# Optimization experiments

Measured on AMD Instinct MI355X. Metric: run time of the kernel, lower is better.

The kernel has to match this reference:

```python
import jax, jax.numpy as jnp
import numpy as np
from functools import partial

C_IN = 32
KT = 10  # 3*3 taps + bias


def avgpool(x, k):
    B, C, H, W = x.shape
    return x.reshape(B, C, H // k, k, W // k, k).mean(axis=(3, 5))


def conv3x3(x, w, b):
    out = jax.lax.conv_general_dilated(
        x, w, window_strides=(1, 1), padding=[(1, 1), (1, 1)],
        dimension_numbers=("NCHW", "OIHW", "NCHW"))
    return out + b[None, :, None, None]


def conv1x1(x, w, b):
    # w: [O, C, 1, 1]
    return jnp.einsum("bchw,oc->bohw", x, w[:, :, 0, 0]) + b[None, :, None, None]


def predictor(x, w1, b1, w2, b2):
    return x + conv3x3(jax.nn.leaky_relu(conv3x3(x, w1, b1), 0.01), w2, b2)


def flying_conv(x, weight, bias):
    # x: [B,C,H,W]; weight: [B,C,Hb,Wb,9]; bias: [B,C,Hb,Wb]; 8x8 blocks
    B, C, H, W = x.shape
    Hb, Wb = H // 8, W // 8
    xp = jnp.pad(x, ((0, 0), (0, 0), (1, 1), (1, 1)))
    out = jnp.broadcast_to(bias[:, :, :, None, :, None], (B, C, Hb, 8, Wb, 8))
    for k in range(9):
        di, dj = k // 3, k % 3
        xs = xp[:, :, di:di + H, dj:dj + W].reshape(B, C, Hb, 8, Wb, 8)
        out = out + xs * weight[:, :, :, None, :, None, k]
    return out.reshape(B, C, H, W)


def setup_inputs() -> dict:
    key = jax.random.key(0)
    ks = jax.random.split(key, 5)
    B, C, H, W = 4, C_IN, 512, 512
    x = jax.random.normal(ks[0], (B, C, H, W), dtype=jnp.float32)
    pa_w = jax.random.normal(ks[1], (4, 2, C, C, 3, 3), dtype=jnp.float32) * 0.05
    pa_b = jnp.zeros((4, 2, C), dtype=jnp.float32)
    exp_w = jax.random.normal(ks[2], (C * KT, C, 1, 1), dtype=jnp.float32) * 0.05
    exp_b = jnp.zeros((C * KT,), dtype=jnp.float32)
    pw_w = jax.random.normal(ks[3], (C, C, 1, 1), dtype=jnp.float32) * 0.1
    pw_b = jnp.zeros((C,), dtype=jnp.float32)
    return {"x": x, "pa_w": pa_w, "pa_b": pa_b, "exp_w": exp_w,
            "exp_b": exp_b, "pw_w": pw_w, "pw_b": pw_b}


def reference(x, pa_w, pa_b, exp_w, exp_b, pw_w, pw_b):
    B, C, H, W = x.shape
    feat = avgpool(x, 4)  # H/4
    for i in range(4):
        feat = predictor(feat, pa_w[i, 0], pa_b[i, 0], pa_w[i, 1], pa_b[i, 1])
        if i == 1:
            feat = avgpool(feat, 2)  # -> H/8
    wmap = conv1x1(feat, exp_w, exp_b)  # [B, C*10, Hb, Wb]
    Hb, Wb = H // 8, W // 8
    wmap = jnp.tanh(wmap.reshape(B, C, KT, Hb, Wb).transpose(0, 1, 3, 4, 2))
    weight, bias = wmap[..., :9], wmap[..., 9]
    out = flying_conv(x, weight, bias)
    return conv1x1(out, pw_w, pw_b)
```

## Files before the change

kernel.cpp:

```cpp
#include <hip/hip_runtime.h>


#define BATCH 4
#define NCH 32
#define CS128 17680
#define SP128 136
#define CS64 4752
#define SP64 72

__device__ __forceinline__ float fast_tanh(float s) {
  float e = __expf(2.f * s);
  return fmaf(-2.f, __builtin_amdgcn_rcpf(e + 1.f), 1.f);
}

__global__ void zero_kernel(float* __restrict__ p) {
  int i = blockIdx.x * 256 + threadIdx.x;
  *reinterpret_cast<float4*>(p + (size_t)i * 4) = make_float4(0.f, 0.f, 0.f, 0.f);
}

__global__ void prep_kernel(const float* __restrict__ pa_w, const float* __restrict__ exp_w,
                            const float* __restrict__ pw_w, float* __restrict__ wt,
                            float* __restrict__ ewt, float* __restrict__ pwt) {
  int i = blockIdx.x * 256 + threadIdx.x;
  if (i < 73728) {
    int tap = i % 9; int t = i / 9;
    int ci = t & 31; t >>= 5;
    int co = t & 31; int layer = t >> 5;
    wt[((layer * 32 + ci) * 9 + tap) * 32 + co] = pa_w[i];
  } else if (i < 83968) {
    int j = i - 73728; int ci = j & 31; int o = j >> 5;
    ewt[ci * 320 + o] = exp_w[j];
  } else if (i < 84992) {
    int j = i - 83968; int c = j & 31; int o = j >> 5;
    pwt[c * 32 + o] = pw_w[j];
  }
}

__global__ void avgpool4_kernel(const float* __restrict__ x, float* __restrict__ outp) {
  int idx = blockIdx.x * 256 + threadIdx.x;
  if (idx >= BATCH * NCH * 128 * 128) return;
  int ow = idx & 127; int t = idx >> 7; int oh = t & 127; int bc = t >> 7;
  const float* src = x + ((size_t)(bc * 512 + oh * 4)) * 512 + ow * 4;
  float s = 0.f;
#pragma unroll
  for (int r = 0; r < 4; r++) {
    float4 v = *reinterpret_cast<const float4*>(src + (size_t)r * 512);
    s += v.x + v.y + v.z + v.w;
  }
  outp[(size_t)bc * CS128 + (size_t)(oh + 1) * SP128 + ow + 4] = s * 0.0625f;
}

__global__ void avgpool2_kernel(const float* __restrict__ inp, float* __restrict__ outp) {
  int idx = blockIdx.x * 256 + threadIdx.x;
  if (idx >= BATCH * NCH * 64 * 64) return;
  int ow = idx & 63; int t = idx >> 6; int oh = t & 63; int bc = t >> 6;
  const float* sp = inp + (size_t)bc * CS128 + (size_t)(2 * oh + 1) * SP128 + 2 * ow + 4;
  float2 a = *reinterpret_cast<const float2*>(sp);
  float2 b = *reinterpret_cast<const float2*>(sp + SP128);
  outp[(size_t)bc * CS64 + (size_t)(oh + 1) * SP64 + ow + 4] = (a.x + a.y + b.x + b.y) * 0.25f;
}

template <int HS, int SP, int CS, int NCO, bool RELU, bool RES>
__global__ __launch_bounds__(256) void conv3x3d_kernel(
    const float* __restrict__ in, const float* __restrict__ wt,
    const float* __restrict__ bias, const float* __restrict__ res,
    float* __restrict__ out) {
  constexpr int TILES = HS / 16;
  constexpr int GROUPS = 32 / NCO;
  int blk = blockIdx.x;
  int g = blk % GROUPS; int rest = blk / GROUPS;
  int b = rest / (TILES * TILES); int t = rest % (TILES * TILES);
  int ty = t / TILES, tx = t % TILES;
  int og = g * NCO;
  int px = threadIdx.x & 15, py = threadIdx.x >> 4;
  int gy = ty * 16 + py, gx = tx * 16 + px;
  size_t pix = (size_t)(gy + 1) * SP + gx + 4;
  const float* inb = in + (size_t)b * 32 * CS + pix;

  float acc[NCO];
#pragma unroll
  for (int o = 0; o < NCO; o++) acc[o] = bias[og + o];

  for (int ci = 0; ci < 32; ci++) {
    const float* p = inb + (size_t)ci * CS;
    float v[9];
    v[0] = p[-SP - 1]; v[1] = p[-SP]; v[2] = p[-SP + 1];
    v[3] = p[-1];      v[4] = p[0];   v[5] = p[1];
    v[6] = p[SP - 1];  v[7] = p[SP];  v[8] = p[SP + 1];
    const float* wr = wt + ci * 288 + og;
#pragma unroll
    for (int tap = 0; tap < 9; tap++) {
      const float* wrow = wr + tap * 32;
#pragma unroll
      for (int o = 0; o < NCO; o++)
        acc[o] = fmaf(v[tap], wrow[o], acc[o]);
    }
  }

  float* ob = out + (size_t)b * 32 * CS + (size_t)og * CS + pix;
  const float* rb = RES ? (res + (size_t)b * 32 * CS + (size_t)og * CS + pix) : nullptr;
#pragma unroll
  for (int o = 0; o < NCO; o++) {
    float r2 = acc[o];
    if (RELU) r2 = r2 > 0.f ? r2 : 0.01f * r2;
    if (RES) r2 += rb[(size_t)o * CS];
    ob[(size_t)o * CS] = r2;
  }
}

__global__ __launch_bounds__(256) void expander_kernel(
    const float* __restrict__ feat, const float* __restrict__ ewt,
    const float* __restrict__ eb, float* __restrict__ wmap) {
  int idx = blockIdx.x * 256 + threadIdx.x;
  int wq = idx & 15; int t = idx >> 4;
  int o = t % 320; int rest = t / 320;
  int hb = rest & 63; int b = rest >> 6;
  const float* fp = feat + (size_t)b * 32 * CS64 + (size_t)(hb + 1) * SP64 + 4 + wq * 4;
  float s0 = eb[o];
  float s1 = s0, s2 = s0, s3 = s0;
#pragma unroll 8
  for (int ci = 0; ci < 32; ci++) {
    float4 f = *reinterpret_cast<const float4*>(fp + (size_t)ci * CS64);
    float wv = ewt[ci * 320 + o];
    s0 = fmaf(f.x, wv, s0); s1 = fmaf(f.y, wv, s1);
    s2 = fmaf(f.z, wv, s2); s3 = fmaf(f.w, wv, s3);
  }
  float4 r;
  r.x = fast_tanh(s0); r.y = fast_tanh(s1);
  r.z = fast_tanh(s2); r.w = fast_tanh(s3);
  *reinterpret_cast<float4*>(wmap + (size_t)((b * 64 + hb) * 320 + o) * 64 + wq * 4) = r;
}

__global__ __launch_bounds__(256, 4) void fused_fly_pw_kernel(
    const float* __restrict__ x, const float* __restrict__ wmap,
    const float* __restrict__ pwt, const float* __restrict__ pw_b,
    float* __restrict__ out, int b0) {
  __shared__ float s_w[8][322];
  __shared__ float s_x[8][10][68];
  int blk = blockIdx.x;
  int wtile = blk & 7; int t = blk >> 3; int hb = t & 63; int b = b0 + (t >> 6);
  int tid = threadIdx.x;

  const float* wsrc = wmap + (size_t)(b * 64 + hb) * 320 * 64 + wtile * 8;
#pragma unroll
  for (int j = 0; j < 10; j++) {
    int idx = j * 256 + tid;
    int tap = idx >> 3, wb8 = idx & 7;
    s_w[wb8][tap] = wsrc[(size_t)tap * 64 + wb8];
  }

  int cp = tid & 31, row = tid >> 5;
  int h = hb * 8 + row;
  int w0 = wtile * 64 + cp * 2;
  int wbl = cp >> 2;
  int h0 = hb * 8;
  int gc0 = wtile * 64 - 1;
  const float* xb = x + (size_t)b * 32 * 262144;

  float2 acc[32];
#pragma unroll
  for (int o = 0; o < 32; o++) {
    float bv = pw_b[o];
    acc[o].x = bv; acc[o].y = bv;
  }

  for (int g = 0; g < 4; g++) {
    __syncthreads();
    const float* xg = xb + (size_t)(g * 8) * 262144;
    for (int e = tid; e < 5280; e += 256) {
      int ch = e / 660; int r2 = e - ch * 660;
      int rr = r2 / 66; int cl = r2 - rr * 66;
      int gy = h0 - 1 + rr, gx = gc0 + cl;
      float v = 0.f;
      if (gy >= 0 && gy < 512 && gx >= 0 && gx < 512)
        v = xg[(size_t)ch * 262144 + (size_t)gy * 512 + gx];
      s_x[ch][rr][cl] = v;
    }
    __syncthreads();

#pragma unroll
    for (int c8 = 0; c8 < 8; c8++) {
      int c = g * 8 + c8;
      const float2* wr2 = reinterpret_cast<const float2*>(&s_w[wbl][c * 10]);
      float2 w01 = wr2[0], w23 = wr2[1], w45 = wr2[2], w67 = wr2[3], w89 = wr2[4];
      float wv[9];
      wv[0] = w01.x; wv[1] = w01.y; wv[2] = w23.x;
      wv[3] = w23.y; wv[4] = w45.x; wv[5] = w45.y;
      wv[6] = w67.x; wv[7] = w67.y; wv[8] = w89.x;
      float fly0 = w89.y, fly1 = w89.y;

#pragma unroll
      for (int di = 0; di < 3; di++) {
        const float2* rp = reinterpret_cast<const float2*>(&s_x[c8][row + di][cp * 2]);
        float2 a = rp[0], bb = rp[1];
        float wa = wv[di * 3 + 0], wb_ = wv[di * 3 + 1], wc = wv[di * 3 + 2];
        fly0 = fmaf(a.x, wa, fly0); fly0 = fmaf(a.y, wb_, fly0); fly0 = fmaf(bb.x, wc, fly0);
        fly1 = fmaf(a.y, wa, fly1); fly1 = fmaf(bb.x, wb_, fly1); fly1 = fmaf(bb.y, wc, fly1);
      }
      const float* prow = pwt + c * 32;
#pragma unroll
      for (int o = 0; o < 32; o++) {
        float pw = prow[o];
        acc[o].x = fmaf(fly0, pw, acc[o].x);
        acc[o].y = fmaf(fly1, pw, acc[o].y);
      }
    }
  }
  float* ob = out + (size_t)b * 32 * 262144 + (size_t)h * 512 + w0;
#pragma unroll
  for (int o = 0; o < 32; o++)
    *reinterpret_cast<float2*>(ob + (size_t)o * 262144) = acc[o];
}

extern "C" void kernel_launch(void* const* d_in, const int* in_sizes, int n_in,
                              void* d_out, int out_size, void* d_ws, size_t ws_size,
                              hipStream_t stream) {
  const float* x     = (const float*)d_in[0];
  const float* pa_w  = (const float*)d_in[1];
  const float* pa_b  = (const float*)d_in[2];
  const float* exp_w = (const float*)d_in[3];
  const float* exp_b = (const float*)d_in[4];
  const float* pw_w  = (const float*)d_in[5];
  const float* pw_b  = (const float*)d_in[6];
  float* out = (float*)d_out;
  float* ws  = (float*)d_ws;

  float* feat0p = ws;
  float* tmpAp  = feat0p + 2263040;
  float* feat1p = tmpAp + 2263040;
  float* wmap   = feat1p + 608256;
  float* tmpBp  = wmap;
  float* wt     = wmap + 5242880;
  float* ewt    = wt + 73728;
  float* pwt    = ewt + 10240;

  hipLaunchKernelGGL(zero_kernel, dim3(5608), dim3(256), 0, stream, ws);
  hipLaunchKernelGGL(prep_kernel, dim3(332), dim3(256), 0, stream, pa_w, exp_w, pw_w, wt, ewt, pwt);
  hipLaunchKernelGGL(avgpool4_kernel, dim3(8192), dim3(256), 0, stream, x, feat0p);

  for (int i = 0; i < 2; i++) {
    const float* w1 = wt + (size_t)(i * 2 + 0) * 9216;
    const float* b1 = pa_b + (i * 2 + 0) * 32;
    const float* w2 = wt + (size_t)(i * 2 + 1) * 9216;
    const float* b2 = pa_b + (i * 2 + 1) * 32;
    hipLaunchKernelGGL((conv3x3d_kernel<128, SP128, CS128, 8, true, false>),
                       dim3(1024), dim3(256), 0, stream, feat0p, w1, b1, nullptr, tmpAp);
    hipLaunchKernelGGL((conv3x3d_kernel<128, SP128, CS128, 8, false, true>),
                       dim3(1024), dim3(256), 0, stream, tmpAp, w2, b2, feat0p, feat0p);
  }

  hipLaunchKernelGGL(avgpool2_kernel, dim3(2048), dim3(256), 0, stream, feat0p, feat1p);

  for (int i = 2; i < 4; i++) {
    const float* w1 = wt + (size_t)(i * 2 + 0) * 9216;
    const float* b1 = pa_b + (i * 2 + 0) * 32;
    const float* w2 = wt + (size_t)(i * 2 + 1) * 9216;
    const float* b2 = pa_b + (i * 2 + 1) * 32;
    hipLaunchKernelGGL((conv3x3d_kernel<64, SP64, CS64, 4, true, false>),
                       dim3(512), dim3(256), 0, stream, feat1p, w1, b1, nullptr, tmpBp);
    hipLaunchKernelGGL((conv3x3d_kernel<64, SP64, CS64, 4, false, true>),
                       dim3(512), dim3(256), 0, stream, tmpBp, w2, b2, feat1p, feat1p);
  }

  hipLaunchKernelGGL(expander_kernel, dim3(5120), dim3(256), 0, stream, feat1p, ewt, exp_b, wmap);

  hipLaunchKernelGGL(fused_fly_pw_kernel, dim3(1024), dim3(256), 0, stream,
                     x, wmap, pwt, pw_b, out, 0);
  hipLaunchKernelGGL(fused_fly_pw_kernel, dim3(1024), dim3(256), 0, stream,
                     x, wmap, pwt, pw_b, out, 2);
}
```

Baseline: 380.4 us.

## Halve per-thread work in conv and fused flying-conv kernels, merge batch launches

```diff
diff --git a/kernel.cpp b/kernel.cpp
--- a/kernel.cpp
+++ b/kernel.cpp
@@ -81,6 +81,7 @@
 #pragma unroll
   for (int o = 0; o < NCO; o++) acc[o] = bias[og + o];
 
+#pragma unroll 2
   for (int ci = 0; ci < 32; ci++) {
     const float* p = inb + (size_t)ci * CS;
     float v[9];
@@ -131,43 +132,40 @@
   *reinterpret_cast<float4*>(wmap + (size_t)((b * 64 + hb) * 320 + o) * 64 + wq * 4) = r;
 }
 
-__global__ __launch_bounds__(256, 4) void fused_fly_pw_kernel(
+__global__ __launch_bounds__(512) void fused_fly_pw_kernel(
     const float* __restrict__ x, const float* __restrict__ wmap,
     const float* __restrict__ pwt, const float* __restrict__ pw_b,
-    float* __restrict__ out, int b0) {
+    float* __restrict__ out) {
   __shared__ float s_w[8][322];
   __shared__ float s_x[8][10][68];
   int blk = blockIdx.x;
-  int wtile = blk & 7; int t = blk >> 3; int hb = t & 63; int b = b0 + (t >> 6);
+  int wtile = blk & 7; int t = blk >> 3; int hb = t & 63; int b = t >> 6;
   int tid = threadIdx.x;
 
   const float* wsrc = wmap + (size_t)(b * 64 + hb) * 320 * 64 + wtile * 8;
 #pragma unroll
-  for (int j = 0; j < 10; j++) {
-    int idx = j * 256 + tid;
+  for (int j = 0; j < 5; j++) {
+    int idx = j * 512 + tid;
     int tap = idx >> 3, wb8 = idx & 7;
     s_w[wb8][tap] = wsrc[(size_t)tap * 64 + wb8];
   }
 
-  int cp = tid & 31, row = tid >> 5;
+  int cp = tid & 63, row = tid >> 6;
   int h = hb * 8 + row;
-  int w0 = wtile * 64 + cp * 2;
-  int wbl = cp >> 2;
+  int w0 = wtile * 64 + cp;
+  int wbl = cp >> 3;
   int h0 = hb * 8;
   int gc0 = wtile * 64 - 1;
   const float* xb = x + (size_t)b * 32 * 262144;
 
-  float2 acc[32];
-#pragma unroll
-  for (int o = 0; o < 32; o++) {
-    float bv = pw_b[o];
-    acc[o].x = bv; acc[o].y = bv;
-  }
+  float acc[32];
+#pragma unroll
+  for (int o = 0; o < 32; o++) acc[o] = pw_b[o];
 
   for (int g = 0; g < 4; g++) {
     __syncthreads();
     const float* xg = xb + (size_t)(g * 8) * 262144;
-    for (int e = tid; e < 5280; e += 256) {
+    for (int e = tid; e < 5280; e += 512) {
       int ch = e / 660; int r2 = e - ch * 660;
       int rr = r2 / 66; int cl = r2 - rr * 66;
       int gy = h0 - 1 + rr, gx = gc0 + cl;
@@ -187,29 +185,25 @@
       wv[0] = w01.x; wv[1] = w01.y; wv[2] = w23.x;
       wv[3] = w23.y; wv[4] = w45.x; wv[5] = w45.y;
       wv[6] = w67.x; wv[7] = w67.y; wv[8] = w89.x;
-      float fly0 = w89.y, fly1 = w89.y;
+      float fly = w89.y;
 
 #pragma unroll
       for (int di = 0; di < 3; di++) {
-        const float2* rp = reinterpret_cast<const float2*>(&s_x[c8][row + di][cp * 2]);
-        float2 a = rp[0], bb = rp[1];
-        float wa = wv[di * 3 + 0], wb_ = wv[di * 3 + 1], wc = wv[di * 3 + 2];
-        fly0 = fmaf(a.x, wa, fly0); fly0 = fmaf(a.y, wb_, fly0); fly0 = fmaf(bb.x, wc, fly0);
-        fly1 = fmaf(a.y, wa, fly1); fly1 = fmaf(bb.x, wb_, fly1); fly1 = fmaf(bb.y, wc, fly1);
+        const float* rp = &s_x[c8][row + di][cp];
+        fly = fmaf(rp[0], wv[di * 3 + 0], fly);
+        fly = fmaf(rp[1], wv[di * 3 + 1], fly);
+        fly = fmaf(rp[2], wv[di * 3 + 2], fly);
       }
       const float* prow = pwt + c * 32;
 #pragma unroll
-      for (int o = 0; o < 32; o++) {
-        float pw = prow[o];
-        acc[o].x = fmaf(fly0, pw, acc[o].x);
-        acc[o].y = fmaf(fly1, pw, acc[o].y);
-      }
+      for (int o = 0; o < 32; o++)
+        acc[o] = fmaf(fly, prow[o], acc[o]);
     }
   }
   float* ob = out + (size_t)b * 32 * 262144 + (size_t)h * 512 + w0;
 #pragma unroll
   for (int o = 0; o < 32; o++)
-    *reinterpret_cast<float2*>(ob + (size_t)o * 262144) = acc[o];
+    ob[(size_t)o * 262144] = acc[o];
 }
 
 extern "C" void kernel_launch(void* const* d_in, const int* in_sizes, int n_in,
@@ -243,10 +237,10 @@
     const float* b1 = pa_b + (i * 2 + 0) * 32;
     const float* w2 = wt + (size_t)(i * 2 + 1) * 9216;
     const float* b2 = pa_b + (i * 2 + 1) * 32;
-    hipLaunchKernelGGL((conv3x3d_kernel<128, SP128, CS128, 8, true, false>),
-                       dim3(1024), dim3(256), 0, stream, feat0p, w1, b1, nullptr, tmpAp);
-    hipLaunchKernelGGL((conv3x3d_kernel<128, SP128, CS128, 8, false, true>),
-                       dim3(1024), dim3(256), 0, stream, tmpAp, w2, b2, feat0p, feat0p);
+    hipLaunchKernelGGL((conv3x3d_kernel<128, SP128, CS128, 4, true, false>),
+                       dim3(2048), dim3(256), 0, stream, feat0p, w1, b1, nullptr, tmpAp);
+    hipLaunchKernelGGL((conv3x3d_kernel<128, SP128, CS128, 4, false, true>),
+                       dim3(2048), dim3(256), 0, stream, tmpAp, w2, b2, feat0p, feat0p);
   }
 
   hipLaunchKernelGGL(avgpool2_kernel, dim3(2048), dim3(256), 0, stream, feat0p, feat1p);
@@ -256,16 +250,14 @@
     const float* b1 = pa_b + (i * 2 + 0) * 32;
     const float* w2 = wt + (size_t)(i * 2 + 1) * 9216;
     const float* b2 = pa_b + (i * 2 + 1) * 32;
-    hipLaunchKernelGGL((conv3x3d_kernel<64, SP64, CS64, 4, true, false>),
-                       dim3(512), dim3(256), 0, stream, feat1p, w1, b1, nullptr, tmpBp);
-    hipLaunchKernelGGL((conv3x3d_kernel<64, SP64, CS64, 4, false, true>),
-                       dim3(512), dim3(256), 0, stream, tmpBp, w2, b2, feat1p, feat1p);
+    hipLaunchKernelGGL((conv3x3d_kernel<64, SP64, CS64, 2, true, false>),
+                       dim3(1024), dim3(256), 0, stream, feat1p, w1, b1, nullptr, tmpBp);
+    hipLaunchKernelGGL((conv3x3d_kernel<64, SP64, CS64, 2, false, true>),
+                       dim3(1024), dim3(256), 0, stream, tmpBp, w2, b2, feat1p, feat1p);
   }
 
   hipLaunchKernelGGL(expander_kernel, dim3(5120), dim3(256), 0, stream, feat1p, ewt, exp_b, wmap);
 
-  hipLaunchKernelGGL(fused_fly_pw_kernel, dim3(1024), dim3(256), 0, stream,
-                     x, wmap, pwt, pw_b, out, 0);
-  hipLaunchKernelGGL(fused_fly_pw_kernel, dim3(1024), dim3(256), 0, stream,
-                     x, wmap, pwt, pw_b, out, 2);
-}
+  hipLaunchKernelGGL(fused_fly_pw_kernel, dim3(2048), dim3(512), 0, stream,
+                     x, wmap, pwt, pw_b, out);
+}
```

New measurement: 373.6 us. No clear change (-1.8%).
